# Performance work log

Hardware: AMD Instinct MI355X
Metric: run time of the kernel (lower is better)

Reference implementation:

```python
import jax, jax.numpy as jnp
import numpy as np

VOCAB, EMBED, HIDDEN = 32000, 100, 100
B, S = 16, 256


def setup_inputs() -> dict:
    key = jax.random.key(0)
    ks = jax.random.split(key, 8)
    std = 1.0 / np.sqrt(HIDDEN)
    u = lambda k, shp: jax.random.uniform(k, shp, jnp.float32, -std, std)
    return {
        "x": jax.random.randint(ks[0], (B, S), 0, VOCAB),
        "hidden": jnp.zeros((B, HIDDEN), jnp.float32),
        "emb": u(ks[1], (VOCAB, EMBED)),
        "W_ih": u(ks[2], (EMBED, HIDDEN)),
        "W_hh": u(ks[3], (HIDDEN, HIDDEN)),
        "b_ih": u(ks[4], (HIDDEN,)),
        "b_hh": u(ks[5], (HIDDEN,)),
        "W_fc": u(ks[6], (HIDDEN, VOCAB)),
        "b_fc": u(ks[7], (VOCAB,)),
    }


def reference(x, hidden, emb, W_ih, W_hh, b_ih, b_hh, W_fc, b_fc):
    # Embedding lookup: [B, S, E]
    embedded = emb[x]

    def step(h_prev, x_t):  # x_t: [B, E], h_prev: [B, H]
        h_t = jnp.tanh(x_t @ W_ih + b_ih + h_prev @ W_hh + b_hh)
        return h_t, h_t

    # scan over time (axis 0 after swap): outputs hs: [S, B, H]
    h_last, hs = jax.lax.scan(step, hidden, jnp.swapaxes(embedded, 0, 1))
    hs = jnp.swapaxes(hs, 0, 1)  # [B, S, H]

    logits = hs @ W_fc + b_fc  # [B, S, V]
    log_probs = jax.nn.log_softmax(logits, axis=-1)
    return log_probs, h_last
```

## Files before the change

### kernel.cpp

```cpp
#include <hip/hip_runtime.h>

#define H 100
#define B 16
#define S 256
#define V 32000
#define NROW (B*S)
#define KP 128

typedef __attribute__((ext_vector_type(8))) short short8;
typedef __attribute__((ext_vector_type(4))) float f32x4;

static __device__ __forceinline__ unsigned short f2bf(float f) {
    unsigned u = __float_as_uint(f);
    u += 0x7FFF + ((u >> 16) & 1);
    return (unsigned short)(u >> 16);
}
static __device__ __forceinline__ unsigned pack2(float a, float b) {
    return (unsigned)f2bf(a) | ((unsigned)f2bf(b) << 16);
}

__global__ __launch_bounds__(128) void k_embed_xpart(
    const int* __restrict__ x, const float* __restrict__ emb,
    const float* __restrict__ Wih, const float* __restrict__ bih,
    const float* __restrict__ bhh, float* __restrict__ xpart,
    float* __restrict__ sumexp)
{
    int r0 = blockIdx.x * 16;
    int j = threadIdx.x;
    __shared__ int toks[16];
    __shared__ __align__(16) float e_s[16][100];
    if (j < 16) { toks[j] = x[r0 + j]; sumexp[r0 + j] = 0.f; }
    __syncthreads();
#pragma unroll
    for (int r = 0; r < 16; r++)
        if (j < H) e_s[r][j] = emb[toks[r] * H + j];
    float wv[H];
    if (j < H) {
#pragma unroll
        for (int k = 0; k < H; k++) wv[k] = Wih[k * H + j];
    }
    __syncthreads();
    if (j >= H) return;
    float bias = bih[j] + bhh[j];
    for (int r = 0; r < 16; r++) {
        const float4* e4 = (const float4*)e_s[r];
        float a0 = bias, a1 = 0.f, a2 = 0.f, a3 = 0.f;
#pragma unroll
        for (int kk = 0; kk < 25; kk++) {
            float4 ev = e4[kk];
            a0 = fmaf(ev.x, wv[4*kk+0], a0);
            a1 = fmaf(ev.y, wv[4*kk+1], a1);
            a2 = fmaf(ev.z, wv[4*kk+2], a2);
            a3 = fmaf(ev.w, wv[4*kk+3], a3);
        }
        xpart[(r0 + r) * H + j] = (a0 + a1) + (a2 + a3);
    }
}

__global__ __launch_bounds__(256) void k_wfcT_scan(
    const float* __restrict__ Wfc, unsigned short* __restrict__ WfcT,
    const float* __restrict__ xpart, const float* __restrict__ h0,
    const float* __restrict__ Whh, unsigned short* __restrict__ hsB,
    float* __restrict__ hlast)
{
    if (blockIdx.x < 125) {
        int v = blockIdx.x * 256 + threadIdx.x;
        float w[100];
#pragma unroll
        for (int k = 0; k < 100; k++) w[k] = Wfc[(long long)k * V + v];
        unsigned* dst = (unsigned*)(WfcT + (long long)v * KP);
#pragma unroll
        for (int q = 0; q < 12; q++) {
            uint4 o;
            o.x = pack2(w[q*8+0], w[q*8+1]);
            o.y = pack2(w[q*8+2], w[q*8+3]);
            o.z = pack2(w[q*8+4], w[q*8+5]);
            o.w = pack2(w[q*8+6], w[q*8+7]);
            *(uint4*)(dst + q*4) = o;
        }
        uint2 t;
        t.x = pack2(w[96], w[97]);
        t.y = pack2(w[98], w[99]);
        *(uint2*)(dst + 48) = t;
        *(uint2*)(dst + 50) = make_uint2(0,0);
        *(uint4*)(dst + 52) = make_uint4(0,0,0,0);
        *(uint4*)(dst + 56) = make_uint4(0,0,0,0);
        *(uint4*)(dst + 60) = make_uint4(0,0,0,0);
        return;
    }

    int b = blockIdx.x - 125;
    int j = threadIdx.x;
    __shared__ __align__(16) float hbuf[2][128];
    float wv[H];
    if (j < H) {
#pragma unroll
        for (int k = 0; k < H; k++) wv[k] = Whh[k * H + j];
        hbuf[0][j] = h0[b * H + j];
    }
    __syncthreads();
    float xp = (j < H) ? xpart[(b * S) * H + j] : 0.f;
    int p = 0;
    for (int t = 0; t < S; t++) {
        float hnew = 0.f;
        if (j < H) {
            const float4* h4 = (const float4*)hbuf[p];
            float a0 = xp, a1 = 0.f, a2 = 0.f, a3 = 0.f;
#pragma unroll
            for (int kk = 0; kk < 25; kk++) {
                float4 hv = h4[kk];
                a0 = fmaf(hv.x, wv[4*kk+0], a0);
                a1 = fmaf(hv.y, wv[4*kk+1], a1);
                a2 = fmaf(hv.z, wv[4*kk+2], a2);
                a3 = fmaf(hv.w, wv[4*kk+3], a3);
            }
            if (t + 1 < S) xp = xpart[(b * S + t + 1) * H + j];
            float acc = (a0 + a1) + (a2 + a3);
            float xc = fminf(fmaxf(acc, -15.f), 15.f);
            float e = __expf(2.f * xc);
            hnew = (e - 1.f) / (e + 1.f);
            hbuf[p ^ 1][j] = hnew;
        }
        if (j < KP) hsB[(b * S + t) * KP + j] = (j < H) ? f2bf(hnew) : (unsigned short)0;
        __syncthreads();
        p ^= 1;
    }
    if (j < H) hlast[b * H + j] = hbuf[p][j];
}

__global__ __launch_bounds__(256) void k_sumexp(
    const unsigned short* __restrict__ hsB, const unsigned short* __restrict__ WfcT,
    const float* __restrict__ bfc, float* __restrict__ sumexp)
{
    int bid = blockIdx.x;
    int lane = threadIdx.x & 63, w = threadIdx.x >> 6;
    int quad = lane >> 4, l15 = lane & 15;
    int r0 = (bid >> 4) * 128 + w * 32;
    int n0 = (bid & 15) * 2000;
    const short8* ap0 = (const short8*)(hsB + (long long)(r0 + l15) * KP + quad * 8);
    const short8* ap1 = (const short8*)(hsB + (long long)(r0 + 16 + l15) * KP + quad * 8);
    short8 a00 = ap0[0], a01 = ap0[4], a02 = ap0[8], a03 = ap0[12];
    short8 a10 = ap1[0], a11 = ap1[4], a12 = ap1[8], a13 = ap1[12];
    float p00=0.f,p01=0.f,p02=0.f,p03=0.f;
    float p10=0.f,p11=0.f,p12=0.f,p13=0.f;
    for (int nt = 0; nt < 125; nt++) {
        int col = n0 + nt * 16 + l15;
        const short8* bptr = (const short8*)(WfcT + (long long)col * KP + quad * 8);
        short8 b0 = bptr[0], b1 = bptr[4], b2 = bptr[8], b3 = bptr[12];
        f32x4 c0 = {0.f,0.f,0.f,0.f}, c1 = {0.f,0.f,0.f,0.f};
        c0 = __builtin_amdgcn_mfma_f32_16x16x32_bf16(a00, b0, c0, 0, 0, 0);
        c0 = __builtin_amdgcn_mfma_f32_16x16x32_bf16(a01, b1, c0, 0, 0, 0);
        c0 = __builtin_amdgcn_mfma_f32_16x16x32_bf16(a02, b2, c0, 0, 0, 0);
        c0 = __builtin_amdgcn_mfma_f32_16x16x32_bf16(a03, b3, c0, 0, 0, 0);
        c1 = __builtin_amdgcn_mfma_f32_16x16x32_bf16(a10, b0, c1, 0, 0, 0);
        c1 = __builtin_amdgcn_mfma_f32_16x16x32_bf16(a11, b1, c1, 0, 0, 0);
        c1 = __builtin_amdgcn_mfma_f32_16x16x32_bf16(a12, b2, c1, 0, 0, 0);
        c1 = __builtin_amdgcn_mfma_f32_16x16x32_bf16(a13, b3, c1, 0, 0, 0);
        float bias = bfc[col];
        p00 += __expf(c0[0] + bias); p01 += __expf(c0[1] + bias);
        p02 += __expf(c0[2] + bias); p03 += __expf(c0[3] + bias);
        p10 += __expf(c1[0] + bias); p11 += __expf(c1[1] + bias);
        p12 += __expf(c1[2] + bias); p13 += __expf(c1[3] + bias);
    }
#pragma unroll
    for (int m = 1; m <= 8; m <<= 1) {
        p00 += __shfl_xor(p00, m); p01 += __shfl_xor(p01, m);
        p02 += __shfl_xor(p02, m); p03 += __shfl_xor(p03, m);
        p10 += __shfl_xor(p10, m); p11 += __shfl_xor(p11, m);
        p12 += __shfl_xor(p12, m); p13 += __shfl_xor(p13, m);
    }
    if (l15 == 0) {
        int rr = r0 + quad * 4;
        atomicAdd(&sumexp[rr + 0], p00);
        atomicAdd(&sumexp[rr + 1], p01);
        atomicAdd(&sumexp[rr + 2], p02);
        atomicAdd(&sumexp[rr + 3], p03);
        atomicAdd(&sumexp[rr + 16], p10);
        atomicAdd(&sumexp[rr + 17], p11);
        atomicAdd(&sumexp[rr + 18], p12);
        atomicAdd(&sumexp[rr + 19], p13);
    }
}

__global__ __launch_bounds__(256) void k_out(
    const unsigned short* __restrict__ hsB, const unsigned short* __restrict__ WfcT,
    const float* __restrict__ bfc, const float* __restrict__ sumexp,
    float* __restrict__ out)
{
    int bid = blockIdx.x;
    int cc = bid >> 4;
    int rt = bid & 15;
    int lane = threadIdx.x & 63, w = threadIdx.x >> 6;
    int quad = lane >> 4, l15 = lane & 15;
    int r0 = rt * 256 + w * 64;
    int n0 = cc * 128;
    short8 a[4][4];
#pragma unroll
    for (int i = 0; i < 4; i++) {
        const short8* ap = (const short8*)(hsB + (long long)(r0 + i * 16 + l15) * KP + quad * 8);
        a[i][0] = ap[0]; a[i][1] = ap[4]; a[i][2] = ap[8]; a[i][3] = ap[12];
    }
    float ls[4][4];
#pragma unroll
    for (int i = 0; i < 4; i++)
#pragma unroll
        for (int jj = 0; jj < 4; jj++)
            ls[i][jj] = __logf(sumexp[r0 + i * 16 + quad * 4 + jj]);
    long long base0 = (long long)(r0 + quad * 4) * V + n0 + l15;
#pragma unroll
    for (int nt = 0; nt < 8; nt++) {
        int col = n0 + nt * 16 + l15;
        const short8* bptr = (const short8*)(WfcT + (long long)col * KP + quad * 8);
        short8 b0 = bptr[0], b1 = bptr[4], b2 = bptr[8], b3 = bptr[12];
        float bias = bfc[col];
#pragma unroll
        for (int i = 0; i < 4; i++) {
            f32x4 c = {0.f,0.f,0.f,0.f};
            c = __builtin_amdgcn_mfma_f32_16x16x32_bf16(a[i][0], b0, c, 0, 0, 0);
            c = __builtin_amdgcn_mfma_f32_16x16x32_bf16(a[i][1], b1, c, 0, 0, 0);
            c = __builtin_amdgcn_mfma_f32_16x16x32_bf16(a[i][2], b2, c, 0, 0, 0);
            c = __builtin_amdgcn_mfma_f32_16x16x32_bf16(a[i][3], b3, c, 0, 0, 0);
            long long rb = base0 + (long long)i * 16 * V + nt * 16;
            out[rb]           = c[0] + bias - ls[i][0];
            out[rb + V]       = c[1] + bias - ls[i][1];
            out[rb + 2LL * V] = c[2] + bias - ls[i][2];
            out[rb + 3LL * V] = c[3] + bias - ls[i][3];
        }
    }
}

extern "C" void kernel_launch(void* const* d_in, const int* in_sizes, int n_in,
                              void* d_out, int out_size, void* d_ws, size_t ws_size,
                              hipStream_t stream)
{
    const int*   x    = (const int*)d_in[0];
    const float* h0   = (const float*)d_in[1];
    const float* emb  = (const float*)d_in[2];
    const float* Wih  = (const float*)d_in[3];
    const float* Whh  = (const float*)d_in[4];
    const float* bih  = (const float*)d_in[5];
    const float* bhh  = (const float*)d_in[6];
    const float* Wfc  = (const float*)d_in[7];
    const float* bfc  = (const float*)d_in[8];

    float* out   = (float*)d_out;
    float* hlast = out + (long long)NROW * V;

    float* xpart  = (float*)d_ws;
    float* sumexp = xpart + NROW * H;
    unsigned short* WfcT = (unsigned short*)(sumexp + NROW);
    unsigned short* hsB  = WfcT + (long long)V * KP;

    k_embed_xpart<<<256, 128, 0, stream>>>(x, emb, Wih, bih, bhh, xpart, sumexp);
    k_wfcT_scan<<<141, 256, 0, stream>>>(Wfc, WfcT, xpart, h0, Whh, hsB, hlast);
    k_sumexp<<<512, 256, 0, stream>>>(hsB, WfcT, bfc, sumexp);
    k_out<<<4000, 256, 0, stream>>>(hsB, WfcT, bfc, sumexp, out);
}
```

Before: 933.2 us.

## Stage W_fc tiles in swizzled LDS and retile sumexp grid; nontemporal output stores

Both GEMM kernels now cooperatively load a 128-column tile of the transposed bf16 W_fc into shared memory with an XOR swizzle and read MFMA B fragments from LDS, instead of each wave reading them from global memory. The sumexp kernel is retiled from 512 blocks, each looping over 2000 columns, to 8000 blocks that each cover 128 columns, which raises parallelism but multiplies the atomic adds into sumexp. Output log-prob stores become nontemporal to avoid polluting the cache with the large 524MB output.

```diff
diff --git a/kernel.cpp b/kernel.cpp
--- a/kernel.cpp
+++ b/kernel.cpp
@@ -17,6 +17,25 @@
 }
 static __device__ __forceinline__ unsigned pack2(float a, float b) {
     return (unsigned)f2bf(a) | ((unsigned)f2bf(b) << 16);
+}
+
+static __device__ __forceinline__ void stage_B128(
+    const unsigned short* __restrict__ WfcT, int n0,
+    unsigned short* Bs, int tid)
+{
+    const uint4* src = (const uint4*)(WfcT + (long long)n0 * KP);
+    uint4* dst = (uint4*)Bs;
+#pragma unroll
+    for (int k = 0; k < 8; k++) {
+        int u = k * 256 + tid;
+        int us = u ^ ((u >> 4) & 7);
+        dst[u] = src[us];
+    }
+}
+static __device__ __forceinline__ short8 bfrag(
+    const unsigned short* Bs, int nt, int l15, int slot)
+{
+    return *(const short8*)(Bs + nt * 2048 + l15 * 128 + ((slot ^ (l15 & 7)) * 8));
 }
 
 __global__ __launch_bounds__(128) void k_embed_xpart(
@@ -132,21 +151,30 @@
     const unsigned short* __restrict__ hsB, const unsigned short* __restrict__ WfcT,
     const float* __restrict__ bfc, float* __restrict__ sumexp)
 {
+    __shared__ __align__(16) unsigned short Bs[128 * KP];
     int bid = blockIdx.x;
-    int lane = threadIdx.x & 63, w = threadIdx.x >> 6;
+    int cc = bid >> 5, rt = bid & 31;
+    int tid = threadIdx.x;
+    int lane = tid & 63, w = tid >> 6;
     int quad = lane >> 4, l15 = lane & 15;
-    int r0 = (bid >> 4) * 128 + w * 32;
-    int n0 = (bid & 15) * 2000;
+    int n0 = cc * 128;
+    int r0 = rt * 128 + w * 32;
+
+    stage_B128(WfcT, n0, Bs, tid);
+
     const short8* ap0 = (const short8*)(hsB + (long long)(r0 + l15) * KP + quad * 8);
     const short8* ap1 = (const short8*)(hsB + (long long)(r0 + 16 + l15) * KP + quad * 8);
     short8 a00 = ap0[0], a01 = ap0[4], a02 = ap0[8], a03 = ap0[12];
     short8 a10 = ap1[0], a11 = ap1[4], a12 = ap1[8], a13 = ap1[12];
     float p00=0.f,p01=0.f,p02=0.f,p03=0.f;
     float p10=0.f,p11=0.f,p12=0.f,p13=0.f;
-    for (int nt = 0; nt < 125; nt++) {
-        int col = n0 + nt * 16 + l15;
-        const short8* bptr = (const short8*)(WfcT + (long long)col * KP + quad * 8);
-        short8 b0 = bptr[0], b1 = bptr[4], b2 = bptr[8], b3 = bptr[12];
+    __syncthreads();
+#pragma unroll
+    for (int nt = 0; nt < 8; nt++) {
+        short8 b0 = bfrag(Bs, nt, l15, quad);
+        short8 b1 = bfrag(Bs, nt, l15, quad + 4);
+        short8 b2 = bfrag(Bs, nt, l15, quad + 8);
+        short8 b3 = bfrag(Bs, nt, l15, quad + 12);
         f32x4 c0 = {0.f,0.f,0.f,0.f}, c1 = {0.f,0.f,0.f,0.f};
         c0 = __builtin_amdgcn_mfma_f32_16x16x32_bf16(a00, b0, c0, 0, 0, 0);
         c0 = __builtin_amdgcn_mfma_f32_16x16x32_bf16(a01, b1, c0, 0, 0, 0);
@@ -156,7 +184,7 @@
         c1 = __builtin_amdgcn_mfma_f32_16x16x32_bf16(a11, b1, c1, 0, 0, 0);
         c1 = __builtin_amdgcn_mfma_f32_16x16x32_bf16(a12, b2, c1, 0, 0, 0);
         c1 = __builtin_amdgcn_mfma_f32_16x16x32_bf16(a13, b3, c1, 0, 0, 0);
-        float bias = bfc[col];
+        float bias = bfc[n0 + nt * 16 + l15];
         p00 += __expf(c0[0] + bias); p01 += __expf(c0[1] + bias);
         p02 += __expf(c0[2] + bias); p03 += __expf(c0[3] + bias);
         p10 += __expf(c1[0] + bias); p11 += __expf(c1[1] + bias);
@@ -187,13 +215,18 @@
     const float* __restrict__ bfc, const float* __restrict__ sumexp,
     float* __restrict__ out)
 {
+    __shared__ __align__(16) unsigned short Bs[128 * KP];
     int bid = blockIdx.x;
     int cc = bid >> 4;
     int rt = bid & 15;
-    int lane = threadIdx.x & 63, w = threadIdx.x >> 6;
+    int tid = threadIdx.x;
+    int lane = tid & 63, w = tid >> 6;
     int quad = lane >> 4, l15 = lane & 15;
     int r0 = rt * 256 + w * 64;
     int n0 = cc * 128;
+
+    stage_B128(WfcT, n0, Bs, tid);
+
     short8 a[4][4];
 #pragma unroll
     for (int i = 0; i < 4; i++) {
@@ -206,13 +239,16 @@
 #pragma unroll
         for (int jj = 0; jj < 4; jj++)
             ls[i][jj] = __logf(sumexp[r0 + i * 16 + quad * 4 + jj]);
+    __syncthreads();
+
     long long base0 = (long long)(r0 + quad * 4) * V + n0 + l15;
 #pragma unroll
     for (int nt = 0; nt < 8; nt++) {
-        int col = n0 + nt * 16 + l15;
-        const short8* bptr = (const short8*)(WfcT + (long long)col * KP + quad * 8);
-        short8 b0 = bptr[0], b1 = bptr[4], b2 = bptr[8], b3 = bptr[12];
-        float bias = bfc[col];
+        short8 b0 = bfrag(Bs, nt, l15, quad);
+        short8 b1 = bfrag(Bs, nt, l15, quad + 4);
+        short8 b2 = bfrag(Bs, nt, l15, quad + 8);
+        short8 b3 = bfrag(Bs, nt, l15, quad + 12);
+        float bias = bfc[n0 + nt * 16 + l15];
 #pragma unroll
         for (int i = 0; i < 4; i++) {
             f32x4 c = {0.f,0.f,0.f,0.f};
@@ -221,10 +257,10 @@
             c = __builtin_amdgcn_mfma_f32_16x16x32_bf16(a[i][2], b2, c, 0, 0, 0);
             c = __builtin_amdgcn_mfma_f32_16x16x32_bf16(a[i][3], b3, c, 0, 0, 0);
             long long rb = base0 + (long long)i * 16 * V + nt * 16;
-            out[rb]           = c[0] + bias - ls[i][0];
-            out[rb + V]       = c[1] + bias - ls[i][1];
-            out[rb + 2LL * V] = c[2] + bias - ls[i][2];
-            out[rb + 3LL * V] = c[3] + bias - ls[i][3];
+            __builtin_nontemporal_store(c[0] + bias - ls[i][0], &out[rb]);
+            __builtin_nontemporal_store(c[1] + bias - ls[i][1], &out[rb + V]);
+            __builtin_nontemporal_store(c[2] + bias - ls[i][2], &out[rb + 2LL * V]);
+            __builtin_nontemporal_store(c[3] + bias - ls[i][3], &out[rb + 3LL * V]);
         }
     }
 }
@@ -253,6 +289,6 @@
 
     k_embed_xpart<<<256, 128, 0, stream>>>(x, emb, Wih, bih, bhh, xpart, sumexp);
     k_wfcT_scan<<<141, 256, 0, stream>>>(Wfc, WfcT, xpart, h0, Whh, hsB, hlast);
-    k_sumexp<<<512, 256, 0, stream>>>(hsB, WfcT, bfc, sumexp);
+    k_sumexp<<<8000, 256, 0, stream>>>(hsB, WfcT, bfc, sumexp);
     k_out<<<4000, 256, 0, stream>>>(hsB, WfcT, bfc, sumexp, out);
 }
```

Result: faster. 862.4 us (-7.6%).
